# Performance work log

Hardware: AMD Instinct MI355X
Metric: run time of the kernel (lower is better)

## Reference

```python
import jax, jax.numpy as jnp
import numpy as np
from jax import lax

D_MODEL = 1024
KERNEL = 7
EPS = 1e-8


def setup_inputs() -> dict:
    key = jax.random.key(0)
    ks = jax.random.split(key, 8)
    B, T, D = 4, 4096, D_MODEL
    x = jax.random.normal(ks[0], (B, T, D), dtype=jnp.float32)
    # rotary tables [T, D/2]
    pos = jnp.arange(T, dtype=jnp.float32)[:, None]
    inv_freq = 1.0 / (10000.0 ** (jnp.arange(D // 2, dtype=jnp.float32) / (D // 2)))
    ang = pos * inv_freq[None, :]
    sin = jnp.sin(ang)
    cos = jnp.cos(ang)
    # params
    W_proj = jax.random.normal(ks[1], (D, 2 * D), dtype=jnp.float32) * (1.0 / np.sqrt(D))
    b_proj = jnp.zeros((2 * D,), dtype=jnp.float32)
    dw_kernel = jax.random.normal(ks[2], (KERNEL, 1, D), dtype=jnp.float32) * 0.1  # [K,1,C] WIO depthwise
    dw_bias = jnp.zeros((D,), dtype=jnp.float32)
    gamma = jnp.ones((D,), dtype=jnp.float32)
    return {"x": x, "sin": sin, "cos": cos, "W_proj": W_proj, "b_proj": b_proj,
            "dw_kernel": dw_kernel, "dw_bias": dw_bias, "gamma": gamma}


def reference(x, sin, cos, W_proj, b_proj, dw_kernel, dw_bias, gamma):
    D = D_MODEL
    proj = jnp.einsum('btd,df->btf', x, W_proj) + b_proj          # [B,T,2D]
    x_a, x_b = proj[..., :D], proj[..., D:]
    # interleaved rotary: even/odd pairs
    x1 = x_a[..., 0::2]                                            # [B,T,D/2]
    x2 = x_a[..., 1::2]
    c = cos[None, :, :]
    s = sin[None, :, :]
    r1 = x1 * c - x2 * s
    r2 = x1 * s + x2 * c
    x_rot = jnp.stack([r1, r2], axis=-1).reshape(x_a.shape)        # re-interleave
    # depthwise conv1d, SAME padding
    conv = lax.conv_general_dilated(
        x_rot, dw_kernel, window_strides=(1,), padding='SAME',
        dimension_numbers=('NWC', 'WIO', 'NWC'), feature_group_count=D) + dw_bias
    act = conv * jax.nn.sigmoid(conv)                              # swish
    gated = act * jax.nn.sigmoid(x_b)
    rms = jnp.sqrt(jnp.mean(jnp.square(gated), axis=-1, keepdims=True) + EPS)
    return gamma * (gated / rms)
```

## Files before the change

### kernel.cpp

```cpp
#include <hip/hip_runtime.h>
#include <stdint.h>

#define D_MODEL 1024
#define T_LEN   4096
#define B_SZ    4
#define NROWS   (B_SZ * T_LEN)
#define NPROJ   (2 * D_MODEL)
#define CHUNK   32

#define BM 256
#define BN 256
#define BK 64
#define NT (D_MODEL / BK)

typedef __attribute__((ext_vector_type(8))) __bf16 bf16x8;
typedef __attribute__((ext_vector_type(4))) float  f32x4;

using as1_void = __attribute__((address_space(1))) void;
using as3_void = __attribute__((address_space(3))) void;

__device__ inline float bf2f(unsigned short u) {
    union { unsigned int i; float f; } v; v.i = ((unsigned int)u) << 16; return v.f;
}
__device__ inline unsigned short f2bf(float f) {
    union { float f; unsigned int i; } v; v.f = f;
    return (unsigned short)((v.i + 0x7fffu + ((v.i >> 16) & 1u)) >> 16);
}
__device__ inline float sigmoidf(float x) { return 1.0f / (1.0f + __expf(-x)); }

__global__ __launch_bounds__(256) void k_cvt(const float* __restrict__ x,
                                             unsigned short* __restrict__ xb,
                                             const float* __restrict__ W,
                                             unsigned short* __restrict__ wt) {
    __shared__ unsigned short tile[32][33];
    int bid = blockIdx.x;
    if (bid < (NROWS * D_MODEL) / (256 * 4)) {
        int i = (bid * 256 + threadIdx.x) * 4;
        float4 v = *reinterpret_cast<const float4*>(x + i);
        ushort4 o;
        o.x = f2bf(v.x); o.y = f2bf(v.y); o.z = f2bf(v.z); o.w = f2bf(v.w);
        *reinterpret_cast<ushort4*>(xb + i) = o;
    } else {
        bid -= (NROWS * D_MODEL) / (256 * 4);
        int n0 = (bid & 63) * 32, k0 = (bid >> 6) * 32;
        int c = threadIdx.x & 31, r = threadIdx.x >> 5;
        #pragma unroll
        for (int i = 0; i < 4; i++) {
            int kk = r + i * 8;
            tile[kk][c] = f2bf(W[(uint64_t)(k0 + kk) * NPROJ + n0 + c]);
        }
        __syncthreads();
        #pragma unroll
        for (int i = 0; i < 4; i++) {
            int nn = r + i * 8;
            wt[(uint64_t)(n0 + nn) * D_MODEL + k0 + c] = tile[c][nn];
        }
    }
}

__global__ __launch_bounds__(512, 2) void k_gemm(const unsigned short* __restrict__ xb,
                                                 const unsigned short* __restrict__ wt,
                                                 const float* __restrict__ bias,
                                                 unsigned short* __restrict__ projb) {
    __shared__ __align__(16) unsigned short As[2 * BM * BK];
    __shared__ __align__(16) unsigned short Bs[2 * BM * BK];

    const int tid  = threadIdx.x;
    const int lane = tid & 63;
    const int w    = tid >> 6;
    const int wm   = w >> 2;
    const int wn   = w & 3;

    const int bid = blockIdx.x;
    const int wg  = (bid & 7) * 64 + (bid >> 3);
    const int n0  = (wg >> 6) * BN;
    const int m0  = (wg & 63) * BM;

    const int srow = tid >> 3;
    const int scol = ((tid & 7) ^ (srow & 7)) * 8;
    const int fr   = lane & 15;
    const int fq   = lane >> 4;

    f32x4 acc[8][4] = {};

    auto STAGE = [&](int buf, int ks) {
        #pragma unroll
        for (int i = 0; i < 4; ++i) {
            const unsigned short* ga = xb + (uint64_t)(m0 + i * 64 + srow) * D_MODEL + ks + scol;
            __builtin_amdgcn_global_load_lds((as1_void*)(void*)ga,
                (as3_void*)(void*)&As[buf * (BM * BK) + i * 4096 + w * 512], 16, 0, 0);
        }
        #pragma unroll
        for (int i = 0; i < 4; ++i) {
            const unsigned short* gb = wt + (uint64_t)(n0 + i * 64 + srow) * D_MODEL + ks + scol;
            __builtin_amdgcn_global_load_lds((as1_void*)(void*)gb,
                (as3_void*)(void*)&Bs[buf * (BM * BK) + i * 4096 + w * 512], 16, 0, 0);
        }
    };

    STAGE(0, 0);
    __syncthreads();

    for (int t = 0; t < NT; ++t) {
        const int cur = t & 1;
        if (t + 1 < NT) STAGE(1 - cur, (t + 1) * BK);

        const unsigned short* Ab = &As[cur * (BM * BK)];
        const unsigned short* Bb = &Bs[cur * (BM * BK)];
        #pragma unroll
        for (int kk = 0; kk < BK; kk += 32) {
            const int slot = (kk >> 3) + fq;
            bf16x8 b[4];
            #pragma unroll
            for (int n = 0; n < 4; n++) {
                const int rb = wn * 64 + n * 16 + fr;
                b[n] = *reinterpret_cast<const bf16x8*>(&Bb[rb * 64 + ((slot ^ (fr & 7)) * 8)]);
            }
            #pragma unroll
            for (int m = 0; m < 8; m++) {
                const int ra = wm * 128 + m * 16 + fr;
                bf16x8 a = *reinterpret_cast<const bf16x8*>(&Ab[ra * 64 + ((slot ^ (fr & 7)) * 8)]);
                #pragma unroll
                for (int n = 0; n < 4; n++)
                    acc[m][n] = __builtin_amdgcn_mfma_f32_16x16x32_bf16(a, b[n], acc[m][n], 0, 0, 0);
            }
        }
        __syncthreads();
    }

    #pragma unroll
    for (int m = 0; m < 8; m++) {
        const int grow = m0 + wm * 128 + m * 16 + fq * 4;
        #pragma unroll
        for (int n = 0; n < 4; n++) {
            const int gcol = n0 + wn * 64 + n * 16 + fr;
            const float bv = bias[gcol];
            #pragma unroll
            for (int r = 0; r < 4; r++) {
                projb[(uint64_t)(grow + r) * NPROJ + gcol] = f2bf(acc[m][n][r] + bv);
            }
        }
    }
}

__global__ __launch_bounds__(512) void k_post(const unsigned short* __restrict__ projb,
                                              const float* __restrict__ kw,
                                              const float* __restrict__ dwb,
                                              const float* __restrict__ gamma,
                                              float* __restrict__ out) {
    const int blk  = blockIdx.x;
    const int b    = blk / (T_LEN / CHUNK);
    const int t0   = (blk % (T_LEN / CHUNK)) * CHUNK;
    const int c    = threadIdx.x;
    const int d0   = c * 2;
    const uint64_t bbase = (uint64_t)b * T_LEN;

    const float invf = exp2f((float)c * (-13.287712379549449f / 512.0f));

    float kwv[7][2];
    #pragma unroll
    for (int j = 0; j < 7; j++) {
        kwv[j][0] = kw[j * D_MODEL + d0];
        kwv[j][1] = kw[j * D_MODEL + d0 + 1];
    }
    const float bv0 = dwb[d0], bv1 = dwb[d0 + 1];
    const float gm0 = gamma[d0], gm1 = gamma[d0 + 1];

    __shared__ float red[2][8];

    auto load_rope = [&](int tj, float& o0, float& o1) {
        if ((unsigned)tj < (unsigned)T_LEN) {
            ushort2 u = *reinterpret_cast<const ushort2*>(projb + (bbase + tj) * NPROJ + d0);
            float sv, cv;
            __sincosf((float)tj * invf, &sv, &cv);
            float x0 = bf2f(u.x), x1 = bf2f(u.y);
            o0 = x0 * cv - x1 * sv;
            o1 = x0 * sv + x1 * cv;
        } else { o0 = 0.f; o1 = 0.f; }
    };

    float rg[6][2];
    #pragma unroll
    for (int j = 0; j < 6; j++) load_rope(t0 - 3 + j, rg[j][0], rg[j][1]);
    float nx0, nx1;
    load_rope(t0 + 3, nx0, nx1);

    ushort2 xb_cur = *reinterpret_cast<const ushort2*>(projb + (bbase + t0) * NPROJ + D_MODEL + d0);

    for (int t = t0; t < t0 + CHUNK; ++t) {
        const float r60 = nx0, r61 = nx1;

        float acc0 = rg[0][0] * kwv[0][0] + rg[1][0] * kwv[1][0] + rg[2][0] * kwv[2][0]
                   + rg[3][0] * kwv[3][0] + rg[4][0] * kwv[4][0] + rg[5][0] * kwv[5][0]
                   + r60 * kwv[6][0] + bv0;
        float acc1 = rg[0][1] * kwv[0][1] + rg[1][1] * kwv[1][1] + rg[2][1] * kwv[2][1]
                   + rg[3][1] * kwv[3][1] + rg[4][1] * kwv[4][1] + rg[5][1] * kwv[5][1]
                   + r61 * kwv[6][1] + bv1;

        load_rope(t + 4, nx0, nx1);
        const ushort2 xb_use = xb_cur;
        if (t + 1 < t0 + CHUNK) {
            xb_cur = *reinterpret_cast<const ushort2*>(projb + (bbase + t + 1) * NPROJ + D_MODEL + d0);
        }

        float a0 = acc0 * sigmoidf(acc0);
        float a1 = acc1 * sigmoidf(acc1);
        float g0 = a0 * sigmoidf(bf2f(xb_use.x));
        float g1 = a1 * sigmoidf(bf2f(xb_use.y));

        float ssq = g0 * g0 + g1 * g1;
        #pragma unroll
        for (int off = 32; off; off >>= 1) ssq += __shfl_down(ssq, off);
        const int p = t & 1;
        if ((threadIdx.x & 63) == 0) red[p][threadIdx.x >> 6] = ssq;
        __syncthreads();
        float total = red[p][0] + red[p][1] + red[p][2] + red[p][3]
                    + red[p][4] + red[p][5] + red[p][6] + red[p][7];
        const float inv = 1.0f / sqrtf(total * (1.0f / (float)D_MODEL) + 1e-8f);

        float2 o;
        o.x = g0 * inv * gm0;
        o.y = g1 * inv * gm1;
        *reinterpret_cast<float2*>(out + (bbase + t) * D_MODEL + d0) = o;

        #pragma unroll
        for (int j = 0; j < 5; j++) { rg[j][0] = rg[j + 1][0]; rg[j][1] = rg[j + 1][1]; }
        rg[5][0] = r60; rg[5][1] = r61;
    }
}

extern "C" void kernel_launch(void* const* d_in, const int* in_sizes, int n_in,
                              void* d_out, int out_size, void* d_ws, size_t ws_size,
                              hipStream_t stream) {
    const float* x     = (const float*)d_in[0];
    const float* sinp  = (const float*)d_in[1];
    const float* cosp  = (const float*)d_in[2];
    const float* W     = (const float*)d_in[3];
    const float* bproj = (const float*)d_in[4];
    const float* dwk   = (const float*)d_in[5];
    const float* dwb   = (const float*)d_in[6];
    const float* gamma = (const float*)d_in[7];
    float* out = (float*)d_out;
    (void)sinp; (void)cosp;

    unsigned short* xb    = (unsigned short*)d_ws;
    unsigned short* wt    = xb + (size_t)NROWS * D_MODEL;
    unsigned short* projb = wt + (size_t)NPROJ * D_MODEL;

    const int cvt_x_blocks = (NROWS * D_MODEL) / (256 * 4);
    const int cvt_w_blocks = (NPROJ / 32) * (D_MODEL / 32);
    k_cvt<<<cvt_x_blocks + cvt_w_blocks, 256, 0, stream>>>(x, xb, W, wt);
    k_gemm<<<(NPROJ / BN) * (NROWS / BM), 512, 0, stream>>>(xb, wt, bproj, projb);
    k_post<<<B_SZ * (T_LEN / CHUNK), 512, 0, stream>>>(projb, dwk, dwb, gamma, out);
}
```

Measured before the change: 153.7 us.

## Batch RMS reductions per chunk to replace per-row block barriers

The epilogue kernel no longer runs a __syncthreads per row. Each thread keeps its gated values for a whole chunk in registers and writes the per-wave partial sums into shared memory. One barrier pass then computes all inverse RMS values before the outputs are written. Chunk size drops from 32 to 16 so the register arrays stay small and more blocks are available. The costs are higher register pressure and more halo reloads per chunk.

```diff
diff --git a/kernel.cpp b/kernel.cpp
--- a/kernel.cpp
+++ b/kernel.cpp
@@ -6,7 +6,7 @@
 #define B_SZ    4
 #define NROWS   (B_SZ * T_LEN)
 #define NPROJ   (2 * D_MODEL)
-#define CHUNK   32
+#define CHUNK   16
 
 #define BM 256
 #define BN 256
@@ -166,7 +166,8 @@
     const float bv0 = dwb[d0], bv1 = dwb[d0 + 1];
     const float gm0 = gamma[d0], gm1 = gamma[d0 + 1];
 
-    __shared__ float red[2][8];
+    __shared__ float partial[CHUNK][8];
+    __shared__ float invr[CHUNK];
 
     auto load_rope = [&](int tj, float& o0, float& o1) {
         if ((unsigned)tj < (unsigned)T_LEN) {
@@ -182,50 +183,54 @@
     float rg[6][2];
     #pragma unroll
     for (int j = 0; j < 6; j++) load_rope(t0 - 3 + j, rg[j][0], rg[j][1]);
-    float nx0, nx1;
-    load_rope(t0 + 3, nx0, nx1);
-
-    ushort2 xb_cur = *reinterpret_cast<const ushort2*>(projb + (bbase + t0) * NPROJ + D_MODEL + d0);
-
-    for (int t = t0; t < t0 + CHUNK; ++t) {
-        const float r60 = nx0, r61 = nx1;
+
+    float ga[CHUNK], gb[CHUNK];
+
+    #pragma unroll
+    for (int r = 0; r < CHUNK; ++r) {
+        float nx0, nx1;
+        load_rope(t0 + r + 3, nx0, nx1);
+        ushort2 xbv = *reinterpret_cast<const ushort2*>(
+            projb + (bbase + t0 + r) * NPROJ + D_MODEL + d0);
 
         float acc0 = rg[0][0] * kwv[0][0] + rg[1][0] * kwv[1][0] + rg[2][0] * kwv[2][0]
                    + rg[3][0] * kwv[3][0] + rg[4][0] * kwv[4][0] + rg[5][0] * kwv[5][0]
-                   + r60 * kwv[6][0] + bv0;
+                   + nx0 * kwv[6][0] + bv0;
         float acc1 = rg[0][1] * kwv[0][1] + rg[1][1] * kwv[1][1] + rg[2][1] * kwv[2][1]
                    + rg[3][1] * kwv[3][1] + rg[4][1] * kwv[4][1] + rg[5][1] * kwv[5][1]
-                   + r61 * kwv[6][1] + bv1;
-
-        load_rope(t + 4, nx0, nx1);
-        const ushort2 xb_use = xb_cur;
-        if (t + 1 < t0 + CHUNK) {
-            xb_cur = *reinterpret_cast<const ushort2*>(projb + (bbase + t + 1) * NPROJ + D_MODEL + d0);
-        }
+                   + nx1 * kwv[6][1] + bv1;
 
         float a0 = acc0 * sigmoidf(acc0);
         float a1 = acc1 * sigmoidf(acc1);
-        float g0 = a0 * sigmoidf(bf2f(xb_use.x));
-        float g1 = a1 * sigmoidf(bf2f(xb_use.y));
+        float g0 = a0 * sigmoidf(bf2f(xbv.x));
+        float g1 = a1 * sigmoidf(bf2f(xbv.y));
+        ga[r] = g0; gb[r] = g1;
 
         float ssq = g0 * g0 + g1 * g1;
         #pragma unroll
         for (int off = 32; off; off >>= 1) ssq += __shfl_down(ssq, off);
-        const int p = t & 1;
-        if ((threadIdx.x & 63) == 0) red[p][threadIdx.x >> 6] = ssq;
-        __syncthreads();
-        float total = red[p][0] + red[p][1] + red[p][2] + red[p][3]
-                    + red[p][4] + red[p][5] + red[p][6] + red[p][7];
-        const float inv = 1.0f / sqrtf(total * (1.0f / (float)D_MODEL) + 1e-8f);
-
+        if ((c & 63) == 0) partial[r][c >> 6] = ssq;
+
+        #pragma unroll
+        for (int j = 0; j < 5; j++) { rg[j][0] = rg[j + 1][0]; rg[j][1] = rg[j + 1][1]; }
+        rg[5][0] = nx0; rg[5][1] = nx1;
+    }
+
+    __syncthreads();
+    if (c < CHUNK) {
+        float s = partial[c][0] + partial[c][1] + partial[c][2] + partial[c][3]
+                + partial[c][4] + partial[c][5] + partial[c][6] + partial[c][7];
+        invr[c] = 1.0f / sqrtf(s * (1.0f / (float)D_MODEL) + 1e-8f);
+    }
+    __syncthreads();
+
+    #pragma unroll
+    for (int r = 0; r < CHUNK; ++r) {
+        const float iv = invr[r];
         float2 o;
-        o.x = g0 * inv * gm0;
-        o.y = g1 * inv * gm1;
-        *reinterpret_cast<float2*>(out + (bbase + t) * D_MODEL + d0) = o;
-
-        #pragma unroll
-        for (int j = 0; j < 5; j++) { rg[j][0] = rg[j + 1][0]; rg[j][1] = rg[j + 1][1]; }
-        rg[5][0] = r60; rg[5][1] = r61;
+        o.x = ga[r] * iv * gm0;
+        o.y = gb[r] * iv * gm1;
+        *reinterpret_cast<float2*>(out + (bbase + t0 + r) * D_MODEL + d0) = o;
     }
 }
 
```

After: 147.6 us. 4.0% less time.
